# Optimization experiments

Hardware: AMD Instinct MI355X
Metric: run time of the kernel (lower is better)

## Reference

```python
import jax, jax.numpy as jnp
import numpy as np

B, S_T, S_S, P, D = 4, 8, 4, 1024, 1024
NUM_REF = 256
NUM_SHARED = 256
TOPK = 4
TEMP = 1.0
STUDENT_FRAMES = [0, 2, 4, 6]          # teacher indices used by student
EXTRA_FRAMES = [1, 3, 5, 7]            # teacher-only frames
SHARED_TEACHER = [2, 4, 6]             # shared frames (student_frame_indices[1:])
W_D1 = W_D2 = W_D3 = 1.0
HUBER_OUTER_BETA = 0.5


def setup_inputs() -> dict:
    key = jax.random.key(0)
    k1, k2, k3, k4 = jax.random.split(key, 4)
    teacher_feats = jax.random.normal(k1, (B, S_T, P, D), dtype=jnp.float32)
    student_feats = jax.random.normal(k2, (B, S_S, P, D), dtype=jnp.float32)
    ref_perm = jax.random.randint(k3, (NUM_REF,), 0, P, dtype=jnp.int32)
    shared_perm = jax.random.randint(k4, (NUM_SHARED,), 0, P, dtype=jnp.int32)
    return {"teacher_feats": teacher_feats, "student_feats": student_feats,
            "ref_perm": ref_perm, "shared_perm": shared_perm}


def _l2_normalize(x, eps=1e-12):
    n = jnp.maximum(jnp.linalg.norm(x, axis=-1, keepdims=True), eps)
    return x / n


def _smooth_l1_zero(x, beta):
    # SmoothL1Loss(x, 0) elementwise
    ax = jnp.abs(x)
    return jnp.where(ax < beta, 0.5 * ax * ax / beta, ax - 0.5 * beta)


def _kl_branch(diff_t, diff_s):
    # KL(softmax(diff_t/T) || softmax(diff_s/T)) over last dim, then outer huber vs 0
    log_p = jax.nn.log_softmax(diff_t / TEMP, axis=-1)
    log_q = jax.nn.log_softmax(diff_s / TEMP, axis=-1)
    kl = jnp.sum(jnp.exp(log_p) * (log_p - log_q), axis=-1)
    return jnp.sum(_smooth_l1_zero(kl, HUBER_OUTER_BETA)), kl.size


def reference(teacher_feats, student_feats, ref_perm, shared_perm):
    sg = jax.lax.stop_gradient
    N = min(NUM_REF, NUM_SHARED)

    # ref frame (teacher idx 0 -> student idx 0), subsampled patches
    ref_t = sg(teacher_feats[:, 0][:, ref_perm, :])          # [B, num_ref, D]
    ref_s = student_feats[:, 0][:, ref_perm, :]

    # teacher-only frames concatenated along patch dim: [B, 4*P, D]
    extra_t = sg(teacher_feats[:, jnp.array(EXTRA_FRAMES)].reshape(B, len(EXTRA_FRAMES) * P, D))

    # cosine-similarity top-k search (selection_mode='topk')
    sim = jnp.einsum('bnd,bmd->bnm', _l2_normalize(ref_t), _l2_normalize(extra_t))
    _, topk_idx = jax.lax.top_k(sim, TOPK)                    # [B, num_ref, topk]
    sim_high = jax.vmap(lambda e, i: e[i])(extra_t, topk_idx)  # [B, num_ref, topk, D]
    sim_high = sg(sim_high)

    rt = ref_t[:, :N, :]
    rs = ref_s[:, :N, :]
    sh = sim_high[:, :N, :, :]

    sum_d1 = jnp.float32(0.0); sum_d2 = jnp.float32(0.0); sum_d3 = jnp.float32(0.0)
    n_d1 = 0; n_d2 = 0; n_d3 = 0

    for t_idx in SHARED_TEACHER:
        s_idx = STUDENT_FRAMES.index(t_idx)
        st = sg(teacher_feats[:, t_idx][:, shared_perm[:N], :])   # [B, N, D]
        ss = student_feats[:, s_idx][:, shared_perm[:N], :]

        # d1: ref - shared
        l1, c1 = _kl_branch(rt - st, rs - ss)
        sum_d1 += l1; n_d1 += c1
        # d2: ref - sim_high
        l2, c2 = _kl_branch(rt[:, :, None, :] - sh, rs[:, :, None, :] - sh)
        sum_d2 += l2; n_d2 += c2
        # d3: shared - sim_high
        l3, c3 = _kl_branch(st[:, :, None, :] - sh, ss[:, :, None, :] - sh)
        sum_d3 += l3; n_d3 += c3

    loss = (W_D1 * sum_d1 / n_d1 + W_D2 * sum_d2 / n_d2 + W_D3 * sum_d3 / n_d3)
    return loss
```

## Files before the change

### kernel.cpp

```cpp
#include <hip/hip_runtime.h>
#include <hip/hip_bf16.h>
#include <math.h>

#define BATCH 4

typedef __bf16 bf16x8 __attribute__((ext_vector_type(8)));
typedef float f32x4 __attribute__((ext_vector_type(4)));

#define LDSTRIDE 40

__global__ __launch_bounds__(256) void convert_kernel(const float* __restrict__ teacher,
                                                      const int* __restrict__ ref_perm,
                                                      __bf16* __restrict__ Abf,
                                                      __bf16* __restrict__ Bbf,
                                                      float* __restrict__ invnorm) {
    int blk = blockIdx.x;
    int b = blk / 4352;
    int r = blk - b * 4352;
    int t = threadIdx.x;
    const float* src;
    __bf16* dst;
    bool isB = (r >= 256);
    if (!isB) {
        src = teacher + (((size_t)b * 8 + 0) * 1024 + ref_perm[r]) * 1024;
        dst = Abf + ((size_t)b * 256 + r) * 1024;
    } else {
        int m = r - 256;
        int frame = 1 + 2 * (m >> 10), p = m & 1023;
        src = teacher + (((size_t)b * 8 + frame) * 1024 + p) * 1024;
        dst = Bbf + ((size_t)b * 4096 + m) * 1024;
    }
    float4 v = ((const float4*)src)[t];
    float scale = 1.0f;
    __shared__ float red[4];
    if (isB) {
        float s = v.x * v.x + v.y * v.y + v.z * v.z + v.w * v.w;
        for (int o = 32; o > 0; o >>= 1) s += __shfl_xor(s, o);
        if ((t & 63) == 0) red[t >> 6] = s;
        __syncthreads();
        float tot = red[0] + red[1] + red[2] + red[3];
        scale = 1.0f / fmaxf(sqrtf(tot), 1e-12f);
        if (t == 0) invnorm[b * 4096 + (r - 256)] = scale;
    }
    __bf16 o4[4] = {(__bf16)(v.x * scale), (__bf16)(v.y * scale),
                    (__bf16)(v.z * scale), (__bf16)(v.w * scale)};
    ((uint2*)dst)[t] = *(uint2*)o4;
}

__global__ __launch_bounds__(256) void mfma_gemm_kernel(const __bf16* __restrict__ Abf,
                                                        const __bf16* __restrict__ Bbf,
                                                        __bf16* __restrict__ scoresb) {
    int mt = blockIdx.x;
    int nt = blockIdx.y;
    int b  = blockIdx.z;
    int t = threadIdx.x;
    int lane = t & 63, wave = t >> 6;
    int wn0 = (wave & 1) * 64;
    int wm0 = (wave >> 1) * 64;
    int l15 = lane & 15, l4 = lane >> 4;

    __shared__ __bf16 As[128 * LDSTRIDE];
    __shared__ __bf16 Bs[128 * LDSTRIDE];

    const __bf16* Ab = Abf + ((size_t)b * 256 + nt * 128) * 1024;
    const __bf16* Bb = Bbf + ((size_t)b * 4096 + mt * 128) * 1024;

    int e0 = t, e1 = t + 256;
    int row0 = e0 >> 2, kc0 = e0 & 3;
    int row1 = e1 >> 2, kc1 = e1 & 3;

    f32x4 acc[4][4] = {};

    for (int k0 = 0; k0 < 1024; k0 += 32) {
        uint4 a0 = *(const uint4*)(Ab + (size_t)row0 * 1024 + k0 + kc0 * 8);
        uint4 a1 = *(const uint4*)(Ab + (size_t)row1 * 1024 + k0 + kc1 * 8);
        uint4 b0 = *(const uint4*)(Bb + (size_t)row0 * 1024 + k0 + kc0 * 8);
        uint4 b1 = *(const uint4*)(Bb + (size_t)row1 * 1024 + k0 + kc1 * 8);
        __syncthreads();
        *(uint4*)(As + row0 * LDSTRIDE + kc0 * 8) = a0;
        *(uint4*)(As + row1 * LDSTRIDE + kc1 * 8) = a1;
        *(uint4*)(Bs + row0 * LDSTRIDE + kc0 * 8) = b0;
        *(uint4*)(Bs + row1 * LDSTRIDE + kc1 * 8) = b1;
        __syncthreads();
        bf16x8 af[4], bfr[4];
#pragma unroll
        for (int i = 0; i < 4; i++) {
            af[i]  = *(const bf16x8*)(As + (wn0 + i * 16 + l15) * LDSTRIDE + l4 * 8);
            bfr[i] = *(const bf16x8*)(Bs + (wm0 + i * 16 + l15) * LDSTRIDE + l4 * 8);
        }
#pragma unroll
        for (int i = 0; i < 4; i++)
#pragma unroll
            for (int j = 0; j < 4; j++)
                acc[i][j] = __builtin_amdgcn_mfma_f32_16x16x32_bf16(af[i], bfr[j], acc[i][j], 0, 0, 0);
    }

    __bf16* outp = scoresb + ((size_t)b * 256 + nt * 128) * 4096 + (size_t)mt * 128;
#pragma unroll
    for (int i = 0; i < 4; i++)
#pragma unroll
        for (int j = 0; j < 4; j++)
#pragma unroll
            for (int r = 0; r < 4; r++) {
                int n = wn0 + i * 16 + l4 * 4 + r;
                int m = wm0 + j * 16 + l15;
                outp[(size_t)n * 4096 + m] = (__bf16)acc[i][j][r];
            }
}

__global__ __launch_bounds__(256) void topk_rescore_kernel(const __bf16* __restrict__ scoresb,
                                                           const float* __restrict__ teacher,
                                                           const int* __restrict__ ref_perm,
                                                           const float* __restrict__ invnorm,
                                                           int* __restrict__ topk) {
    int row = blockIdx.x;
    int b = row >> 8, n = row & 255;
    int t = threadIdx.x;
    int lane = t & 63, wave = t >> 6;

    __shared__ float refr[1024];
    __shared__ float cval[32];
    __shared__ int cidx[32];
    __shared__ float exact_v[8];
    __shared__ int exact_i[8];

    const float* Tb = teacher + (size_t)b * 8 * 1024 * 1024;
    int rp = ref_perm[n];
    ((float4*)refr)[t] = ((const float4*)(Tb + (size_t)rp * 1024))[t];

    const __bf16* srow = scoresb + (size_t)row * 4096;
    float x[16];
#pragma unroll
    for (int jj = 0; jj < 16; jj++) x[jj] = (float)srow[t + 256 * jj];

    float v[8]; int ix[8];
#pragma unroll
    for (int i = 0; i < 8; i++) { v[i] = -1e38f; ix[i] = -1; }
#pragma unroll
    for (int jj = 0; jj < 16; jj++) {
        float xv = x[jj]; int xm = t + 256 * jj;
        if (xv > v[7]) {
            v[7] = xv; ix[7] = xm;
#pragma unroll
            for (int i = 7; i > 0; i--)
                if (v[i] > v[i - 1]) {
                    float tv = v[i]; v[i] = v[i - 1]; v[i - 1] = tv;
                    int ti = ix[i]; ix[i] = ix[i - 1]; ix[i - 1] = ti;
                }
        }
    }
    for (int r = 0; r < 8; r++) {
        float bv = v[0]; int bi = ix[0];
        for (int o = 32; o > 0; o >>= 1) {
            float ov = __shfl_xor(bv, o); int oi = __shfl_xor(bi, o);
            if (ov > bv || (ov == bv && oi > bi)) { bv = ov; bi = oi; }
        }
        if (lane == 0) { cval[wave * 8 + r] = bv; cidx[wave * 8 + r] = bi; }
        if (bi == ix[0]) {
            v[0] = v[1]; ix[0] = ix[1];
            v[1] = v[2]; ix[1] = ix[2];
            v[2] = v[3]; ix[2] = ix[3];
            v[3] = v[4]; ix[3] = ix[4];
            v[4] = v[5]; ix[4] = ix[5];
            v[5] = v[6]; ix[5] = ix[6];
            v[6] = v[7]; ix[6] = ix[7];
            v[7] = -1e38f; ix[7] = -1;
        }
    }
    __syncthreads();
    if (wave == 0) {
        float mv = (lane < 32) ? cval[lane] : -1e38f;
        int mi = (lane < 32) ? cidx[lane] : -1;
        for (int r = 0; r < 8; r++) {
            float bv = mv; int bi = mi;
            for (int o = 32; o > 0; o >>= 1) {
                float ov = __shfl_xor(bv, o); int oi = __shfl_xor(bi, o);
                if (ov > bv || (ov == bv && oi > bi)) { bv = ov; bi = oi; }
            }
            if (lane == 0) exact_i[r] = bi;
            if (bi == mi) mv = -1e38f;
        }
    }
    __syncthreads();
    for (int c = wave; c < 8; c += 4) {
        int m = exact_i[c];
        int frame = 1 + 2 * (m >> 10), p = m & 1023;
        const float* ext = Tb + ((size_t)frame * 1024 + p) * 1024;
        float s = 0.f;
#pragma unroll
        for (int jj = 0; jj < 16; jj++) {
            int d = lane + 64 * jj;
            s = fmaf(refr[d], ext[d], s);
        }
        for (int o = 32; o > 0; o >>= 1) s += __shfl_xor(s, o);
        if (lane == 0) exact_v[c] = s * invnorm[b * 4096 + m];
    }
    __syncthreads();
    if (t == 0) {
        unsigned used = 0;
        for (int r = 0; r < 4; r++) {
            float bv = -1e38f; int bc = 0;
            for (int c = 0; c < 8; c++)
                if (!(used & (1u << c)) && exact_v[c] > bv) { bv = exact_v[c]; bc = c; }
            used |= 1u << bc;
            topk[row * 4 + r] = exact_i[bc];
        }
    }
}

__global__ __launch_bounds__(256) void kl_kernel(const float* __restrict__ teacher,
                                                 const float* __restrict__ student,
                                                 const int* __restrict__ ref_perm,
                                                 const int* __restrict__ shared_perm,
                                                 const int* __restrict__ topk,
                                                 float* __restrict__ acc) {
    int row = blockIdx.x;
    int b = row >> 8;
    int n = row & 255;
    int t = threadIdx.x;
    int lane = t & 63, wave = t >> 6;

    __shared__ float rt[1024], rs[1024], st[1024], ss[1024];
    __shared__ float sh[4][1024];
    __shared__ float res3[3];
    if (t < 3) res3[t] = 0.f;

    const float* Tb = teacher + (size_t)b * 8 * 1024 * 1024;
    const float* Sb = student + (size_t)b * 4 * 1024 * 1024;

    int rp = ref_perm[n];
    ((float4*)rt)[t] = ((const float4*)(Tb + (size_t)rp * 1024))[t];
    ((float4*)rs)[t] = ((const float4*)(Sb + (size_t)rp * 1024))[t];
#pragma unroll
    for (int k = 0; k < 4; k++) {
        int idx = topk[row * 4 + k];
        int frame = 1 + 2 * (idx >> 10), p = idx & 1023;
        ((float4*)sh[k])[t] = ((const float4*)(Tb + ((size_t)frame * 1024 + p) * 1024))[t];
    }
    int sp = shared_perm[n];

    for (int ti = 0; ti < 3; ti++) {
        int t_idx = 2 * ti + 2;
        int s_idx = ti + 1;
        __syncthreads();
        ((float4*)st)[t] = ((const float4*)(Tb + ((size_t)t_idx * 1024 + sp) * 1024))[t];
        ((float4*)ss)[t] = ((const float4*)(Sb + ((size_t)s_idx * 1024 + sp) * 1024))[t];
        __syncthreads();

        for (int r = wave; r < 9; r += 4) {
            const float *At, *Bt, *Asx, *Bsx;
            int branch;
            if (r == 0)      { At = rt; Bt = st;        Asx = rs; Bsx = ss;        branch = 0; }
            else if (r < 5)  { At = rt; Bt = sh[r - 1]; Asx = rs; Bsx = sh[r - 1]; branch = 1; }
            else             { At = st; Bt = sh[r - 5]; Asx = ss; Bsx = sh[r - 5]; branch = 2; }

            float dt[16], ds[16];
            float mt = -1e38f, ms = -1e38f;
#pragma unroll
            for (int j = 0; j < 16; j++) {
                int d = lane + 64 * j;
                dt[j] = At[d] - Bt[d];
                ds[j] = Asx[d] - Bsx[d];
                mt = fmaxf(mt, dt[j]);
                ms = fmaxf(ms, ds[j]);
            }
            for (int o = 32; o > 0; o >>= 1) {
                mt = fmaxf(mt, __shfl_xor(mt, o));
                ms = fmaxf(ms, __shfl_xor(ms, o));
            }
            float Zt = 0.f, Zs = 0.f, Tn = 0.f;
#pragma unroll
            for (int j = 0; j < 16; j++) {
                float et = __expf(dt[j] - mt);
                Zt += et;
                Zs += __expf(ds[j] - ms);
                Tn += et * (dt[j] - ds[j]);
            }
            for (int o = 32; o > 0; o >>= 1) {
                Zt += __shfl_xor(Zt, o);
                Zs += __shfl_xor(Zs, o);
                Tn += __shfl_xor(Tn, o);
            }
            if (lane == 0) {
                float kl = Tn / Zt - mt - __logf(Zt) + ms + __logf(Zs);
                float ax = fabsf(kl);
                float h = ax < 0.5f ? ax * ax : ax - 0.25f;
                atomicAdd(&res3[branch], h);
            }
        }
    }
    __syncthreads();
    if (t < 3) atomicAdd(&acc[t], res3[t]);
}

__global__ void finalize_kernel(const float* __restrict__ acc, float* __restrict__ out) {
    out[0] = acc[0] / 3072.f + acc[1] / 12288.f + acc[2] / 12288.f;
}

extern "C" void kernel_launch(void* const* d_in, const int* in_sizes, int n_in,
                              void* d_out, int out_size, void* d_ws, size_t ws_size,
                              hipStream_t stream) {
    const float* teacher = (const float*)d_in[0];
    const float* student = (const float*)d_in[1];
    const int* ref_perm = (const int*)d_in[2];
    const int* shared_perm = (const int*)d_in[3];
    float* out = (float*)d_out;

    char* ws = (char*)d_ws;
    float* acc     = (float*)ws;
    float* invnorm = (float*)(ws + 64);
    int*   topk    = (int*)(ws + 64 + 65536);
    __bf16* Abf    = (__bf16*)(ws + 64 + 65536 + 16384);
    __bf16* Bbf    = Abf + (size_t)4 * 256 * 1024;
    __bf16* scoresb = Bbf + (size_t)4 * 4096 * 1024;

    hipMemsetAsync(acc, 0, 64, stream);

    convert_kernel<<<BATCH * 4352, 256, 0, stream>>>(teacher, ref_perm, Abf, Bbf, invnorm);
    mfma_gemm_kernel<<<dim3(32, 2, 4), 256, 0, stream>>>(Abf, Bbf, scoresb);
    topk_rescore_kernel<<<1024, 256, 0, stream>>>(scoresb, teacher, ref_perm, invnorm, topk);
    kl_kernel<<<1024, 256, 0, stream>>>(teacher, student, ref_perm, shared_perm, topk, acc);
    finalize_kernel<<<1, 1, 0, stream>>>(acc, out);
}
```

Before: 282.4 us.

## Fuse top-k rescore with KL kernel and widen GEMM to 512 threads

Merges the top-k rescoring and KL-loss kernels into one, so the eight candidate rows are loaded into shared memory once and reused for both exact rescoring and the KL branches, with no topk round trip through global memory. The GEMM block grows to 8 waves, each computing a 64x32 sub-tile, which raises occupancy but cuts per-wave reuse. The accumulator memset moves into the convert kernel, and score rows are read with vectorized contiguous loads. The fused kernel needs about 50KB of shared memory, which may limit occupancy.

```diff
diff --git a/kernel.cpp b/kernel.cpp
--- a/kernel.cpp
+++ b/kernel.cpp
@@ -13,11 +13,13 @@
                                                       const int* __restrict__ ref_perm,
                                                       __bf16* __restrict__ Abf,
                                                       __bf16* __restrict__ Bbf,
-                                                      float* __restrict__ invnorm) {
+                                                      float* __restrict__ invnorm,
+                                                      float* __restrict__ acc) {
     int blk = blockIdx.x;
     int b = blk / 4352;
     int r = blk - b * 4352;
     int t = threadIdx.x;
+    if (blk == 0 && t < 4) acc[t] = 0.f;
     const float* src;
     __bf16* dst;
     bool isB = (r >= 256);
@@ -47,7 +49,7 @@
     ((uint2*)dst)[t] = *(uint2*)o4;
 }
 
-__global__ __launch_bounds__(256) void mfma_gemm_kernel(const __bf16* __restrict__ Abf,
+__global__ __launch_bounds__(512) void mfma_gemm_kernel(const __bf16* __restrict__ Abf,
                                                         const __bf16* __restrict__ Bbf,
                                                         __bf16* __restrict__ scoresb) {
     int mt = blockIdx.x;
@@ -56,7 +58,7 @@
     int t = threadIdx.x;
     int lane = t & 63, wave = t >> 6;
     int wn0 = (wave & 1) * 64;
-    int wm0 = (wave >> 1) * 64;
+    int wm0 = (wave >> 1) * 32;
     int l15 = lane & 15, l4 = lane >> 4;
 
     __shared__ __bf16 As[128 * LDSTRIDE];
@@ -65,33 +67,28 @@
     const __bf16* Ab = Abf + ((size_t)b * 256 + nt * 128) * 1024;
     const __bf16* Bb = Bbf + ((size_t)b * 4096 + mt * 128) * 1024;
 
-    int e0 = t, e1 = t + 256;
-    int row0 = e0 >> 2, kc0 = e0 & 3;
-    int row1 = e1 >> 2, kc1 = e1 & 3;
-
-    f32x4 acc[4][4] = {};
+    int row0 = t >> 2, kc0 = t & 3;
+
+    f32x4 acc[4][2] = {};
 
     for (int k0 = 0; k0 < 1024; k0 += 32) {
         uint4 a0 = *(const uint4*)(Ab + (size_t)row0 * 1024 + k0 + kc0 * 8);
-        uint4 a1 = *(const uint4*)(Ab + (size_t)row1 * 1024 + k0 + kc1 * 8);
         uint4 b0 = *(const uint4*)(Bb + (size_t)row0 * 1024 + k0 + kc0 * 8);
-        uint4 b1 = *(const uint4*)(Bb + (size_t)row1 * 1024 + k0 + kc1 * 8);
         __syncthreads();
         *(uint4*)(As + row0 * LDSTRIDE + kc0 * 8) = a0;
-        *(uint4*)(As + row1 * LDSTRIDE + kc1 * 8) = a1;
         *(uint4*)(Bs + row0 * LDSTRIDE + kc0 * 8) = b0;
-        *(uint4*)(Bs + row1 * LDSTRIDE + kc1 * 8) = b1;
-        __syncthreads();
-        bf16x8 af[4], bfr[4];
-#pragma unroll
-        for (int i = 0; i < 4; i++) {
-            af[i]  = *(const bf16x8*)(As + (wn0 + i * 16 + l15) * LDSTRIDE + l4 * 8);
-            bfr[i] = *(const bf16x8*)(Bs + (wm0 + i * 16 + l15) * LDSTRIDE + l4 * 8);
-        }
+        __syncthreads();
+        bf16x8 af[4], bfr[2];
 #pragma unroll
         for (int i = 0; i < 4; i++)
-#pragma unroll
-            for (int j = 0; j < 4; j++)
+            af[i] = *(const bf16x8*)(As + (wn0 + i * 16 + l15) * LDSTRIDE + l4 * 8);
+#pragma unroll
+        for (int j = 0; j < 2; j++)
+            bfr[j] = *(const bf16x8*)(Bs + (wm0 + j * 16 + l15) * LDSTRIDE + l4 * 8);
+#pragma unroll
+        for (int i = 0; i < 4; i++)
+#pragma unroll
+            for (int j = 0; j < 2; j++)
                 acc[i][j] = __builtin_amdgcn_mfma_f32_16x16x32_bf16(af[i], bfr[j], acc[i][j], 0, 0, 0);
     }
 
@@ -99,7 +96,7 @@
 #pragma unroll
     for (int i = 0; i < 4; i++)
 #pragma unroll
-        for (int j = 0; j < 4; j++)
+        for (int j = 0; j < 2; j++)
 #pragma unroll
             for (int r = 0; r < 4; r++) {
                 int n = wn0 + i * 16 + l4 * 4 + r;
@@ -108,37 +105,46 @@
             }
 }
 
-__global__ __launch_bounds__(256) void topk_rescore_kernel(const __bf16* __restrict__ scoresb,
-                                                           const float* __restrict__ teacher,
-                                                           const int* __restrict__ ref_perm,
-                                                           const float* __restrict__ invnorm,
-                                                           int* __restrict__ topk) {
+__global__ __launch_bounds__(256) void topk_kl_kernel(const __bf16* __restrict__ scoresb,
+                                                      const float* __restrict__ teacher,
+                                                      const float* __restrict__ student,
+                                                      const int* __restrict__ ref_perm,
+                                                      const int* __restrict__ shared_perm,
+                                                      const float* __restrict__ invnorm,
+                                                      float* __restrict__ acc) {
     int row = blockIdx.x;
     int b = row >> 8, n = row & 255;
     int t = threadIdx.x;
     int lane = t & 63, wave = t >> 6;
 
-    __shared__ float refr[1024];
+    __shared__ float rt[1024], rs[1024], st[1024], ss[1024];
+    __shared__ float sh8[8][1024];
     __shared__ float cval[32];
     __shared__ int cidx[32];
+    __shared__ int cand_i[8];
     __shared__ float exact_v[8];
-    __shared__ int exact_i[8];
+    __shared__ int wslot[4];
+    __shared__ float res3[3];
+    if (t < 3) res3[t] = 0.f;
 
     const float* Tb = teacher + (size_t)b * 8 * 1024 * 1024;
+    const float* Sb = student + (size_t)b * 4 * 1024 * 1024;
+
     int rp = ref_perm[n];
-    ((float4*)refr)[t] = ((const float4*)(Tb + (size_t)rp * 1024))[t];
+    ((float4*)rt)[t] = ((const float4*)(Tb + (size_t)rp * 1024))[t];
+    ((float4*)rs)[t] = ((const float4*)(Sb + (size_t)rp * 1024))[t];
 
     const __bf16* srow = scoresb + (size_t)row * 4096;
-    float x[16];
-#pragma unroll
-    for (int jj = 0; jj < 16; jj++) x[jj] = (float)srow[t + 256 * jj];
+    __bf16 xs[16];
+    *(uint4*)xs = ((const uint4*)srow)[2 * t];
+    *(uint4*)(xs + 8) = ((const uint4*)srow)[2 * t + 1];
 
     float v[8]; int ix[8];
 #pragma unroll
     for (int i = 0; i < 8; i++) { v[i] = -1e38f; ix[i] = -1; }
 #pragma unroll
     for (int jj = 0; jj < 16; jj++) {
-        float xv = x[jj]; int xm = t + 256 * jj;
+        float xv = (float)xs[jj]; int xm = t * 16 + jj;
         if (xv > v[7]) {
             v[7] = xv; ix[7] = xm;
 #pragma unroll
@@ -177,23 +183,27 @@
                 float ov = __shfl_xor(bv, o); int oi = __shfl_xor(bi, o);
                 if (ov > bv || (ov == bv && oi > bi)) { bv = ov; bi = oi; }
             }
-            if (lane == 0) exact_i[r] = bi;
+            if (lane == 0) cand_i[r] = bi;
             if (bi == mi) mv = -1e38f;
         }
     }
     __syncthreads();
+#pragma unroll
+    for (int c = 0; c < 8; c++) {
+        int m = cand_i[c];
+        int frame = 1 + 2 * (m >> 10), p = m & 1023;
+        ((float4*)sh8[c])[t] = ((const float4*)(Tb + ((size_t)frame * 1024 + p) * 1024))[t];
+    }
+    __syncthreads();
     for (int c = wave; c < 8; c += 4) {
-        int m = exact_i[c];
-        int frame = 1 + 2 * (m >> 10), p = m & 1023;
-        const float* ext = Tb + ((size_t)frame * 1024 + p) * 1024;
         float s = 0.f;
 #pragma unroll
         for (int jj = 0; jj < 16; jj++) {
             int d = lane + 64 * jj;
-            s = fmaf(refr[d], ext[d], s);
+            s = fmaf(rt[d], sh8[c][d], s);
         }
         for (int o = 32; o > 0; o >>= 1) s += __shfl_xor(s, o);
-        if (lane == 0) exact_v[c] = s * invnorm[b * 4096 + m];
+        if (lane == 0) exact_v[c] = s * invnorm[b * 4096 + cand_i[c]];
     }
     __syncthreads();
     if (t == 0) {
@@ -203,42 +213,13 @@
             for (int c = 0; c < 8; c++)
                 if (!(used & (1u << c)) && exact_v[c] > bv) { bv = exact_v[c]; bc = c; }
             used |= 1u << bc;
-            topk[row * 4 + r] = exact_i[bc];
-        }
-    }
-}
-
-__global__ __launch_bounds__(256) void kl_kernel(const float* __restrict__ teacher,
-                                                 const float* __restrict__ student,
-                                                 const int* __restrict__ ref_perm,
-                                                 const int* __restrict__ shared_perm,
-                                                 const int* __restrict__ topk,
-                                                 float* __restrict__ acc) {
-    int row = blockIdx.x;
-    int b = row >> 8;
-    int n = row & 255;
-    int t = threadIdx.x;
-    int lane = t & 63, wave = t >> 6;
-
-    __shared__ float rt[1024], rs[1024], st[1024], ss[1024];
-    __shared__ float sh[4][1024];
-    __shared__ float res3[3];
-    if (t < 3) res3[t] = 0.f;
-
-    const float* Tb = teacher + (size_t)b * 8 * 1024 * 1024;
-    const float* Sb = student + (size_t)b * 4 * 1024 * 1024;
-
-    int rp = ref_perm[n];
-    ((float4*)rt)[t] = ((const float4*)(Tb + (size_t)rp * 1024))[t];
-    ((float4*)rs)[t] = ((const float4*)(Sb + (size_t)rp * 1024))[t];
-#pragma unroll
-    for (int k = 0; k < 4; k++) {
-        int idx = topk[row * 4 + k];
-        int frame = 1 + 2 * (idx >> 10), p = idx & 1023;
-        ((float4*)sh[k])[t] = ((const float4*)(Tb + ((size_t)frame * 1024 + p) * 1024))[t];
-    }
+            wslot[r] = bc;
+        }
+    }
+    __syncthreads();
+    const float* shp[4] = {sh8[wslot[0]], sh8[wslot[1]], sh8[wslot[2]], sh8[wslot[3]]};
+
     int sp = shared_perm[n];
-
     for (int ti = 0; ti < 3; ti++) {
         int t_idx = 2 * ti + 2;
         int s_idx = ti + 1;
@@ -250,9 +231,9 @@
         for (int r = wave; r < 9; r += 4) {
             const float *At, *Bt, *Asx, *Bsx;
             int branch;
-            if (r == 0)      { At = rt; Bt = st;        Asx = rs; Bsx = ss;        branch = 0; }
-            else if (r < 5)  { At = rt; Bt = sh[r - 1]; Asx = rs; Bsx = sh[r - 1]; branch = 1; }
-            else             { At = st; Bt = sh[r - 5]; Asx = ss; Bsx = sh[r - 5]; branch = 2; }
+            if (r == 0)      { At = rt; Bt = st;         Asx = rs; Bsx = ss;         branch = 0; }
+            else if (r < 5)  { At = rt; Bt = shp[r - 1]; Asx = rs; Bsx = shp[r - 1]; branch = 1; }
+            else             { At = st; Bt = shp[r - 5]; Asx = ss; Bsx = shp[r - 5]; branch = 2; }
 
             float dt[16], ds[16];
             float mt = -1e38f, ms = -1e38f;
@@ -309,16 +290,12 @@
     char* ws = (char*)d_ws;
     float* acc     = (float*)ws;
     float* invnorm = (float*)(ws + 64);
-    int*   topk    = (int*)(ws + 64 + 65536);
     __bf16* Abf    = (__bf16*)(ws + 64 + 65536 + 16384);
     __bf16* Bbf    = Abf + (size_t)4 * 256 * 1024;
     __bf16* scoresb = Bbf + (size_t)4 * 4096 * 1024;
 
-    hipMemsetAsync(acc, 0, 64, stream);
-
-    convert_kernel<<<BATCH * 4352, 256, 0, stream>>>(teacher, ref_perm, Abf, Bbf, invnorm);
-    mfma_gemm_kernel<<<dim3(32, 2, 4), 256, 0, stream>>>(Abf, Bbf, scoresb);
-    topk_rescore_kernel<<<1024, 256, 0, stream>>>(scoresb, teacher, ref_perm, invnorm, topk);
-    kl_kernel<<<1024, 256, 0, stream>>>(teacher, student, ref_perm, shared_perm, topk, acc);
+    convert_kernel<<<BATCH * 4352, 256, 0, stream>>>(teacher, ref_perm, Abf, Bbf, invnorm, acc);
+    mfma_gemm_kernel<<<dim3(32, 2, 4), 512, 0, stream>>>(Abf, Bbf, scoresb);
+    topk_kl_kernel<<<1024, 256, 0, stream>>>(scoresb, teacher, student, ref_perm, shared_perm, invnorm, acc);
     finalize_kernel<<<1, 1, 0, stream>>>(acc, out);
 }
```

Result: slower. 293.4 us (+3.9%).

## Compute ref-simhigh KL branch once, fold memset into convert, vectorize score loads

Applied to the files above, without the earlier changes.

The d2 KL branch (ref minus sim_high) is identical for all three shared frames, so it is now evaluated only on the first frame and weighted by three. This removes redundant softmax/KL work in the KL kernel. The accumulator zeroing moves into the convert kernel to drop a memset launch, and the topk kernel reads bf16 scores with 16-byte vector loads using a contiguous index mapping. Per-frame load imbalance across waves changes slightly, and summation order differs.

```diff
diff --git a/kernel.cpp b/kernel.cpp
--- a/kernel.cpp
+++ b/kernel.cpp
@@ -13,11 +13,13 @@
                                                       const int* __restrict__ ref_perm,
                                                       __bf16* __restrict__ Abf,
                                                       __bf16* __restrict__ Bbf,
-                                                      float* __restrict__ invnorm) {
+                                                      float* __restrict__ invnorm,
+                                                      float* __restrict__ acc) {
     int blk = blockIdx.x;
     int b = blk / 4352;
     int r = blk - b * 4352;
     int t = threadIdx.x;
+    if (blk == 0 && t < 4) acc[t] = 0.f;
     const float* src;
     __bf16* dst;
     bool isB = (r >= 256);
@@ -121,24 +123,24 @@
     __shared__ float refr[1024];
     __shared__ float cval[32];
     __shared__ int cidx[32];
+    __shared__ int cand_i[8];
     __shared__ float exact_v[8];
-    __shared__ int exact_i[8];
 
     const float* Tb = teacher + (size_t)b * 8 * 1024 * 1024;
     int rp = ref_perm[n];
     ((float4*)refr)[t] = ((const float4*)(Tb + (size_t)rp * 1024))[t];
 
     const __bf16* srow = scoresb + (size_t)row * 4096;
-    float x[16];
-#pragma unroll
-    for (int jj = 0; jj < 16; jj++) x[jj] = (float)srow[t + 256 * jj];
+    __bf16 xs[16];
+    *(uint4*)xs = ((const uint4*)srow)[2 * t];
+    *(uint4*)(xs + 8) = ((const uint4*)srow)[2 * t + 1];
 
     float v[8]; int ix[8];
 #pragma unroll
     for (int i = 0; i < 8; i++) { v[i] = -1e38f; ix[i] = -1; }
 #pragma unroll
     for (int jj = 0; jj < 16; jj++) {
-        float xv = x[jj]; int xm = t + 256 * jj;
+        float xv = (float)xs[jj]; int xm = t * 16 + jj;
         if (xv > v[7]) {
             v[7] = xv; ix[7] = xm;
 #pragma unroll
@@ -177,13 +179,13 @@
                 float ov = __shfl_xor(bv, o); int oi = __shfl_xor(bi, o);
                 if (ov > bv || (ov == bv && oi > bi)) { bv = ov; bi = oi; }
             }
-            if (lane == 0) exact_i[r] = bi;
+            if (lane == 0) cand_i[r] = bi;
             if (bi == mi) mv = -1e38f;
         }
     }
     __syncthreads();
     for (int c = wave; c < 8; c += 4) {
-        int m = exact_i[c];
+        int m = cand_i[c];
         int frame = 1 + 2 * (m >> 10), p = m & 1023;
         const float* ext = Tb + ((size_t)frame * 1024 + p) * 1024;
         float s = 0.f;
@@ -203,7 +205,7 @@
             for (int c = 0; c < 8; c++)
                 if (!(used & (1u << c)) && exact_v[c] > bv) { bv = exact_v[c]; bc = c; }
             used |= 1u << bc;
-            topk[row * 4 + r] = exact_i[bc];
+            topk[row * 4 + r] = cand_i[bc];
         }
     }
 }
@@ -247,11 +249,14 @@
         ((float4*)ss)[t] = ((const float4*)(Sb + ((size_t)s_idx * 1024 + sp) * 1024))[t];
         __syncthreads();
 
-        for (int r = wave; r < 9; r += 4) {
+        int nrows = (ti == 0) ? 9 : 5;
+        for (int idx = wave; idx < nrows; idx += 4) {
+            int r = (ti == 0) ? idx : (idx == 0 ? 0 : idx + 4);
             const float *At, *Bt, *Asx, *Bsx;
             int branch;
+            float w = 1.f;
             if (r == 0)      { At = rt; Bt = st;        Asx = rs; Bsx = ss;        branch = 0; }
-            else if (r < 5)  { At = rt; Bt = sh[r - 1]; Asx = rs; Bsx = sh[r - 1]; branch = 1; }
+            else if (r < 5)  { At = rt; Bt = sh[r - 1]; Asx = rs; Bsx = sh[r - 1]; branch = 1; w = 3.f; }
             else             { At = st; Bt = sh[r - 5]; Asx = ss; Bsx = sh[r - 5]; branch = 2; }
 
             float dt[16], ds[16];
@@ -285,7 +290,7 @@
                 float kl = Tn / Zt - mt - __logf(Zt) + ms + __logf(Zs);
                 float ax = fabsf(kl);
                 float h = ax < 0.5f ? ax * ax : ax - 0.25f;
-                atomicAdd(&res3[branch], h);
+                atomicAdd(&res3[branch], h * w);
             }
         }
     }
@@ -314,9 +319,7 @@
     __bf16* Bbf    = Abf + (size_t)4 * 256 * 1024;
     __bf16* scoresb = Bbf + (size_t)4 * 4096 * 1024;
 
-    hipMemsetAsync(acc, 0, 64, stream);
-
-    convert_kernel<<<BATCH * 4352, 256, 0, stream>>>(teacher, ref_perm, Abf, Bbf, invnorm);
+    convert_kernel<<<BATCH * 4352, 256, 0, stream>>>(teacher, ref_perm, Abf, Bbf, invnorm, acc);
     mfma_gemm_kernel<<<dim3(32, 2, 4), 256, 0, stream>>>(Abf, Bbf, scoresb);
     topk_rescore_kernel<<<1024, 256, 0, stream>>>(scoresb, teacher, ref_perm, invnorm, topk);
     kl_kernel<<<1024, 256, 0, stream>>>(teacher, student, ref_perm, shared_perm, topk, acc);
```

New measurement: 276.8 us. -2.0%, faster.
